# Kernel optimization log

Measured on AMD Instinct MI355X. Metric: run time of the kernel, lower is better.

The kernel has to match this reference:

```python
import jax, jax.numpy as jnp
import numpy as np

NUM_ROUTING = 3
EPS = 1e-7  # keras.backend.epsilon()


def squash(x, axis=-1):
    # squash(s) = (||s||^2 / (1 + ||s||^2)) * s / ||s||, stabilized
    n2 = jnp.sum(x * x, axis=axis, keepdims=True)
    return (n2 / (1.0 + n2)) * x / jnp.sqrt(n2 + EPS)


def setup_inputs() -> dict:
    key = jax.random.key(0)
    k1, k2 = jax.random.split(key)
    B, N_IN, N_OUT, D = 32, 2048, 64, 16
    inputs = jax.random.normal(k1, (B, N_IN, N_OUT, D), dtype=jnp.float32)
    bias = jax.random.normal(k2, (N_OUT, D), dtype=jnp.float32) * 0.01
    return {"inputs": inputs, "bias": bias}


def reference(inputs, bias):
    # inputs: [b, n_in, n_out, d_out]; bias: [n_out, d_out]
    priors = jnp.zeros_like(inputs)
    outputs = None
    for i in range(NUM_ROUTING):
        agreements = jax.nn.softmax(priors, axis=2)           # over n_out
        outputs = jnp.sum(inputs * agreements, axis=1, keepdims=True)  # [b,1,n_out,d]
        outputs = squash(outputs + bias)                       # activation='linear' -> plain squash
        if i < NUM_ROUTING - 1:
            # agreement update, broadcast over d_out
            priors = priors + jnp.sum(inputs * outputs, axis=-1, keepdims=True)
    # reduce '... n_in n_out d_out -> ... n_out d_out' (n_in axis has size 1 here)
    return jnp.sum(outputs, axis=1)
```

## Files before the change

### kernel.cpp

```cpp
#include <hip/hip_runtime.h>
#include <math.h>

#define BB 32
#define NIN 2048
#define NOUT 64
#define DD 16
#define CH 16
#define RPC 128
#define TPB 512

typedef float    f4 __attribute__((ext_vector_type(4)));
typedef float    f8 __attribute__((ext_vector_type(8)));
typedef _Float16 h4 __attribute__((ext_vector_type(4)));
typedef _Float16 h8 __attribute__((ext_vector_type(8)));

__device__ __forceinline__ float dot8(f8 a, f8 b) {
    float s01 = fmaf(a[1], b[1], a[0] * b[0]);
    float s23 = fmaf(a[3], b[3], a[2] * b[2]);
    float s45 = fmaf(a[5], b[5], a[4] * b[4]);
    float s67 = fmaf(a[7], b[7], a[6] * b[6]);
    return (s01 + s23) + (s45 + s67);
}

__global__ __launch_bounds__(TPB, 4) void pass0_kernel(
    const float* __restrict__ x, h4* __restrict__ xh, f4* __restrict__ pout)
{
    const int blk  = blockIdx.x;
    const int chunk = blk & (CH - 1);
    const int b    = blk >> 4;
    const int tid  = threadIdx.x;
    const int lane = tid & 63, wave = tid >> 6;

    f4 acc[4];
    #pragma unroll
    for (int j = 0; j < 4; ++j) acc[j] = f4{0.f, 0.f, 0.f, 0.f};

    const size_t row0 = (size_t)b * NIN + (size_t)chunk * RPC;

    #pragma unroll 2
    for (int r = wave; r < RPC; r += 8) {
        const f4* rp = (const f4*)x + (row0 + r) * 256;
        h4* hp = xh + (row0 + r) * 256;
        #pragma unroll
        for (int j = 0; j < 4; ++j) {
            f4 xv = __builtin_nontemporal_load(&rp[j * 64 + lane]);
            acc[j] += xv;
            hp[j * 64 + lane] = __builtin_convertvector(xv, h4);
        }
    }

    __shared__ f4 red[8][256];
    #pragma unroll
    for (int j = 0; j < 4; ++j) red[wave][j * 64 + lane] = acc[j];
    __syncthreads();
    if (tid < 256) {
        f4 s = red[0][tid];
        #pragma unroll
        for (int w = 1; w < 8; ++w) s += red[w][tid];
        pout[((size_t)(b * CH + chunk)) * 256 + tid] = s;
    }
}

__device__ __forceinline__ void compute_v(
    const f4* __restrict__ pin, const float* __restrict__ bias,
    int b, int tid, float scale, float* vsm, float* vout, int dowrite)
{
    if (tid < 256) {
        f4 s = pin[((size_t)b * CH) * 256 + tid];
        #pragma unroll
        for (int c = 1; c < CH; ++c) s += pin[((size_t)(b * CH + c)) * 256 + tid];
        const f4 bi = ((const f4*)bias)[tid];
        s = s * scale + bi;
        float n2 = s.x * s.x + s.y * s.y + s.z * s.z + s.w * s.w;
        n2 += __shfl_xor(n2, 1);
        n2 += __shfl_xor(n2, 2);
        const float k = n2 / ((1.0f + n2) * sqrtf(n2 + 1e-7f));
        const f4 v = s * k;
        *(f4*)(vsm + tid * 4) = v;
        if (dowrite) ((f4*)vout)[b * 256 + tid] = v;
    }
    __syncthreads();
}

template <int MODE>
__global__ __launch_bounds__(TPB, 4) void pass_kernel(
    const h8* __restrict__ xh,
    const f4* __restrict__ pin,
    const float* __restrict__ bias,
    const float* __restrict__ v0g,
    float* __restrict__ v0out,
    f4* __restrict__ pout)
{
    const int blk  = blockIdx.x;
    const int chunk = blk & (CH - 1);
    const int b    = blk >> 4;
    const int tid  = threadIdx.x;
    const int lane = tid & 63, wave = tid >> 6;

    __shared__ __align__(32) float vsm[1024];
    __shared__ __align__(32) float wsm[1024];
    __shared__ f4 red[8][256];

    const size_t row0 = (size_t)b * NIN + (size_t)chunk * RPC;

    const h8* hp0 = xh + (row0 + wave) * 128;
    h8 hx0 = hp0[lane];
    h8 hx1 = hp0[64 + lane];

    if (MODE == 1) {
        compute_v(pin, bias, b, tid, 1.0f / 64.0f, vsm, v0out, chunk == 0);
    } else {
        if (tid < 256) *(f4*)(vsm + tid * 4) = ((const f4*)v0g)[b * 256 + tid];
        compute_v(pin, bias, b, tid, 1.0f, wsm, nullptr, 0);
    }

    f8 vaf[2];
    #pragma unroll
    for (int j = 0; j < 2; ++j) {
        const int idx = j * 64 + lane;
        vaf[j] = *(const f8*)(vsm + idx * 8);
        if (MODE == 2) vaf[j] += *(const f8*)(wsm + idx * 8);
    }

    f8 acc0 = {0.f, 0.f, 0.f, 0.f, 0.f, 0.f, 0.f, 0.f};
    f8 acc1 = acc0;

    #pragma unroll 2
    for (int r = wave; r < RPC; r += 8) {
        const f8 x0 = __builtin_convertvector(hx0, f8);
        const f8 x1 = __builtin_convertvector(hx1, f8);
        if (r + 8 < RPC) {
            const h8* np = xh + (row0 + r + 8) * 128;
            hx0 = np[lane];
            hx1 = np[64 + lane];
        }

        float d0 = dot8(x0, vaf[0]);
        float d1 = dot8(x1, vaf[1]);
        d0 += __shfl_xor(d0, 1);
        d1 += __shfl_xor(d1, 1);

        const float e0 = __expf(d0), e1 = __expf(d1);
        float p = e0 + e1;
        #pragma unroll
        for (int o = 2; o <= 32; o <<= 1) p += __shfl_xor(p, o);
        const float inv = __builtin_amdgcn_rcpf(p);
        const float a0 = e0 * inv, a1 = e1 * inv;
        #pragma unroll
        for (int k = 0; k < 8; ++k) acc0[k] = fmaf(x0[k], a0, acc0[k]);
        #pragma unroll
        for (int k = 0; k < 8; ++k) acc1[k] = fmaf(x1[k], a1, acc1[k]);
    }

    *(f8*)(&red[wave][lane * 2])       = acc0;
    *(f8*)(&red[wave][128 + lane * 2]) = acc1;
    __syncthreads();
    if (tid < 256) {
        f4 s = red[0][tid];
        #pragma unroll
        for (int w = 1; w < 8; ++w) s += red[w][tid];
        pout[((size_t)(b * CH + chunk)) * 256 + tid] = s;
    }
}

__global__ __launch_bounds__(256) void finish_kernel(
    const f4* __restrict__ pin, const float* __restrict__ bias, f4* __restrict__ out)
{
    const int b = blockIdx.x;
    const int tid = threadIdx.x;
    f4 s = pin[((size_t)b * CH) * 256 + tid];
    #pragma unroll
    for (int c = 1; c < CH; ++c) s += pin[((size_t)(b * CH + c)) * 256 + tid];
    s = s + ((const f4*)bias)[tid];
    float n2 = s.x * s.x + s.y * s.y + s.z * s.z + s.w * s.w;
    n2 += __shfl_xor(n2, 1);
    n2 += __shfl_xor(n2, 2);
    const float k = n2 / ((1.0f + n2) * sqrtf(n2 + 1e-7f));
    out[b * 256 + tid] = s * k;
}

extern "C" void kernel_launch(void* const* d_in, const int* in_sizes, int n_in,
                              void* d_out, int out_size, void* d_ws, size_t ws_size,
                              hipStream_t stream) {
    const float* x    = (const float*)d_in[0];
    const float* bias = (const float*)d_in[1];
    float* out        = (float*)d_out;

    const size_t XH_BYTES = (size_t)BB * NIN * 1024 * 2;
    h4*    xh = (h4*)d_ws;
    float* pA = (float*)((char*)d_ws + XH_BYTES);
    float* pB = pA + (size_t)BB * CH * 1024;
    float* pC = pB + (size_t)BB * CH * 1024;
    float* v0buf = pC + (size_t)BB * CH * 1024;

    pass0_kernel<<<BB * CH, TPB, 0, stream>>>(x, xh, (f4*)pA);
    pass_kernel<1><<<BB * CH, TPB, 0, stream>>>((const h8*)xh, (const f4*)pA, bias,
                                                nullptr, v0buf, (f4*)pB);
    pass_kernel<2><<<BB * CH, TPB, 0, stream>>>((const h8*)xh, (const f4*)pB, bias,
                                                v0buf, nullptr, (f4*)pC);
    finish_kernel<<<BB, 256, 0, stream>>>((const f4*)pC, bias, (f4*)out);
}
```

Before: 116.4 us.

## Split routing passes into two batch halves with smaller blocks for cache residency

Runs the three routing passes separately for each half of the batch (16 samples at a time). The aim is to keep that half's fp16 copy of the inputs (about 64 MB) resident in the last-level cache between passes. Blocks shrink to 256 threads with 64 rows each, and chunks per sample double to 32, giving more blocks per launch. In exchange there are twice as many kernel launches, and compute_v now sums twice as many partial results.

Measured after the change: 135.7 us. 1.17x slower.

```diff
diff --git a/kernel.cpp b/kernel.cpp
--- a/kernel.cpp
+++ b/kernel.cpp
@@ -2,12 +2,13 @@
 #include <math.h>
 
 #define BB 32
+#define HB 16
 #define NIN 2048
 #define NOUT 64
 #define DD 16
-#define CH 16
-#define RPC 128
-#define TPB 512
+#define CH 32
+#define RPC 64
+#define TPB 256
 
 typedef float    f4 __attribute__((ext_vector_type(4)));
 typedef float    f8 __attribute__((ext_vector_type(8)));
@@ -23,13 +24,13 @@
 }
 
 __global__ __launch_bounds__(TPB, 4) void pass0_kernel(
-    const float* __restrict__ x, h4* __restrict__ xh, f4* __restrict__ pout)
+    const float* __restrict__ x, h4* __restrict__ xh, f4* __restrict__ pout, int b0)
 {
-    const int blk  = blockIdx.x;
+    const int blk   = blockIdx.x;
     const int chunk = blk & (CH - 1);
-    const int b    = blk >> 4;
-    const int tid  = threadIdx.x;
-    const int lane = tid & 63, wave = tid >> 6;
+    const int b     = b0 + (blk >> 5);
+    const int tid   = threadIdx.x;
+    const int lane  = tid & 63, wave = tid >> 6;
 
     f4 acc[4];
     #pragma unroll
@@ -38,7 +39,7 @@
     const size_t row0 = (size_t)b * NIN + (size_t)chunk * RPC;
 
     #pragma unroll 2
-    for (int r = wave; r < RPC; r += 8) {
+    for (int r = wave; r < RPC; r += 4) {
         const f4* rp = (const f4*)x + (row0 + r) * 256;
         h4* hp = xh + (row0 + r) * 256;
         #pragma unroll
@@ -49,36 +50,30 @@
         }
     }
 
-    __shared__ f4 red[8][256];
+    __shared__ f4 red[4][256];
     #pragma unroll
     for (int j = 0; j < 4; ++j) red[wave][j * 64 + lane] = acc[j];
     __syncthreads();
-    if (tid < 256) {
-        f4 s = red[0][tid];
-        #pragma unroll
-        for (int w = 1; w < 8; ++w) s += red[w][tid];
-        pout[((size_t)(b * CH + chunk)) * 256 + tid] = s;
-    }
+    f4 s = (red[0][tid] + red[1][tid]) + (red[2][tid] + red[3][tid]);
+    pout[((size_t)(b * CH + chunk)) * 256 + tid] = s;
 }
 
 __device__ __forceinline__ void compute_v(
     const f4* __restrict__ pin, const float* __restrict__ bias,
     int b, int tid, float scale, float* vsm, float* vout, int dowrite)
 {
-    if (tid < 256) {
-        f4 s = pin[((size_t)b * CH) * 256 + tid];
-        #pragma unroll
-        for (int c = 1; c < CH; ++c) s += pin[((size_t)(b * CH + c)) * 256 + tid];
-        const f4 bi = ((const f4*)bias)[tid];
-        s = s * scale + bi;
-        float n2 = s.x * s.x + s.y * s.y + s.z * s.z + s.w * s.w;
-        n2 += __shfl_xor(n2, 1);
-        n2 += __shfl_xor(n2, 2);
-        const float k = n2 / ((1.0f + n2) * sqrtf(n2 + 1e-7f));
-        const f4 v = s * k;
-        *(f4*)(vsm + tid * 4) = v;
-        if (dowrite) ((f4*)vout)[b * 256 + tid] = v;
-    }
+    f4 s = pin[((size_t)b * CH) * 256 + tid];
+    #pragma unroll
+    for (int c = 1; c < CH; ++c) s += pin[((size_t)(b * CH + c)) * 256 + tid];
+    const f4 bi = ((const f4*)bias)[tid];
+    s = s * scale + bi;
+    float n2 = s.x * s.x + s.y * s.y + s.z * s.z + s.w * s.w;
+    n2 += __shfl_xor(n2, 1);
+    n2 += __shfl_xor(n2, 2);
+    const float k = n2 / ((1.0f + n2) * sqrtf(n2 + 1e-7f));
+    const f4 v = s * k;
+    *(f4*)(vsm + tid * 4) = v;
+    if (dowrite) ((f4*)vout)[b * 256 + tid] = v;
     __syncthreads();
 }
 
@@ -89,17 +84,17 @@
     const float* __restrict__ bias,
     const float* __restrict__ v0g,
     float* __restrict__ v0out,
-    f4* __restrict__ pout)
+    f4* __restrict__ pout, int b0)
 {
-    const int blk  = blockIdx.x;
+    const int blk   = blockIdx.x;
     const int chunk = blk & (CH - 1);
-    const int b    = blk >> 4;
-    const int tid  = threadIdx.x;
-    const int lane = tid & 63, wave = tid >> 6;
+    const int b     = b0 + (blk >> 5);
+    const int tid   = threadIdx.x;
+    const int lane  = tid & 63, wave = tid >> 6;
 
     __shared__ __align__(32) float vsm[1024];
     __shared__ __align__(32) float wsm[1024];
-    __shared__ f4 red[8][256];
+    __shared__ f4 red[4][256];
 
     const size_t row0 = (size_t)b * NIN + (size_t)chunk * RPC;
 
@@ -110,7 +105,7 @@
     if (MODE == 1) {
         compute_v(pin, bias, b, tid, 1.0f / 64.0f, vsm, v0out, chunk == 0);
     } else {
-        if (tid < 256) *(f4*)(vsm + tid * 4) = ((const f4*)v0g)[b * 256 + tid];
+        *(f4*)(vsm + tid * 4) = ((const f4*)v0g)[b * 256 + tid];
         compute_v(pin, bias, b, tid, 1.0f, wsm, nullptr, 0);
     }
 
@@ -126,11 +121,11 @@
     f8 acc1 = acc0;
 
     #pragma unroll 2
-    for (int r = wave; r < RPC; r += 8) {
+    for (int r = wave; r < RPC; r += 4) {
         const f8 x0 = __builtin_convertvector(hx0, f8);
         const f8 x1 = __builtin_convertvector(hx1, f8);
-        if (r + 8 < RPC) {
-            const h8* np = xh + (row0 + r + 8) * 128;
+        if (r + 4 < RPC) {
+            const h8* np = xh + (row0 + r + 4) * 128;
             hx0 = np[lane];
             hx1 = np[64 + lane];
         }
@@ -155,12 +150,8 @@
     *(f8*)(&red[wave][lane * 2])       = acc0;
     *(f8*)(&red[wave][128 + lane * 2]) = acc1;
     __syncthreads();
-    if (tid < 256) {
-        f4 s = red[0][tid];
-        #pragma unroll
-        for (int w = 1; w < 8; ++w) s += red[w][tid];
-        pout[((size_t)(b * CH + chunk)) * 256 + tid] = s;
-    }
+    f4 s = (red[0][tid] + red[1][tid]) + (red[2][tid] + red[3][tid]);
+    pout[((size_t)(b * CH + chunk)) * 256 + tid] = s;
 }
 
 __global__ __launch_bounds__(256) void finish_kernel(
@@ -193,10 +184,15 @@
     float* pC = pB + (size_t)BB * CH * 1024;
     float* v0buf = pC + (size_t)BB * CH * 1024;
 
-    pass0_kernel<<<BB * CH, TPB, 0, stream>>>(x, xh, (f4*)pA);
-    pass_kernel<1><<<BB * CH, TPB, 0, stream>>>((const h8*)xh, (const f4*)pA, bias,
-                                                nullptr, v0buf, (f4*)pB);
-    pass_kernel<2><<<BB * CH, TPB, 0, stream>>>((const h8*)xh, (const f4*)pB, bias,
-                                                v0buf, nullptr, (f4*)pC);
+    const int HGRID = HB * CH;
+
+    for (int h = 0; h < 2; ++h) {
+        const int b0 = h * HB;
+        pass0_kernel<<<HGRID, TPB, 0, stream>>>(x, xh, (f4*)pA, b0);
+        pass_kernel<1><<<HGRID, TPB, 0, stream>>>((const h8*)xh, (const f4*)pA, bias,
+                                                  nullptr, v0buf, (f4*)pB, b0);
+        pass_kernel<2><<<HGRID, TPB, 0, stream>>>((const h8*)xh, (const f4*)pB, bias,
+                                                  v0buf, nullptr, (f4*)pC, b0);
+    }
     finish_kernel<<<BB, 256, 0, stream>>>((const f4*)pC, bias, (f4*)out);
 }
```

## Fuse per-batch squash into last-block tail via atomic counters, drop finish kernel

Applied to the files above, without the earlier changes.

Each pass kernel now writes its partial sums with atomic stores and increments a per-batch counter, and the last-arriving block for that batch reduces all chunks, applies bias and squash, and writes v. This replaces the old scheme in which every block of the next kernel re-reduced all 16 partials redundantly, and it removes the separate finish kernel launch. In exchange it adds a memset launch, atomic traffic and a serialized tail on one block per batch.

Result: slower. 179.8 us (+54.5%).

```diff
diff --git a/kernel.cpp b/kernel.cpp
--- a/kernel.cpp
+++ b/kernel.cpp
@@ -3,16 +3,24 @@
 
 #define BB 32
 #define NIN 2048
-#define NOUT 64
-#define DD 16
 #define CH 16
 #define RPC 128
 #define TPB 512
+#define NW 8
 
 typedef float    f4 __attribute__((ext_vector_type(4)));
 typedef float    f8 __attribute__((ext_vector_type(8)));
 typedef _Float16 h4 __attribute__((ext_vector_type(4)));
 typedef _Float16 h8 __attribute__((ext_vector_type(8)));
+
+#define AS __HIP_MEMORY_SCOPE_AGENT
+
+__device__ __forceinline__ void ast(float* p, float v) {
+    __hip_atomic_store(p, v, __ATOMIC_RELAXED, AS);
+}
+__device__ __forceinline__ float ald(const float* p) {
+    return __hip_atomic_load((float*)p, __ATOMIC_RELAXED, AS);
+}
 
 __device__ __forceinline__ float dot8(f8 a, f8 b) {
     float s01 = fmaf(a[1], b[1], a[0] * b[0]);
@@ -22,13 +30,52 @@
     return (s01 + s23) + (s45 + s67);
 }
 
+__device__ __forceinline__ void tail_reduce(
+    f4* red, float* pX, int* cnt, const float* bias,
+    float* vdst, float scale, bool plainOut, int b, int blk, int tid)
+{
+    __syncthreads();
+    if (tid < 256) {
+        f4 s = (red[tid] + red[256 + tid]) + (red[512 + tid] + red[768 + tid]);
+        s += (red[1024 + tid] + red[1280 + tid]) + (red[1536 + tid] + red[1792 + tid]);
+        float* dst = pX + (size_t)blk * 1024 + tid * 4;
+        ast(dst, s.x); ast(dst + 1, s.y); ast(dst + 2, s.z); ast(dst + 3, s.w);
+    }
+    __syncthreads();
+    __shared__ int sLast;
+    if (tid == 0)
+        sLast = (__hip_atomic_fetch_add(&cnt[b], 1, __ATOMIC_ACQ_REL, AS) == CH - 1);
+    __syncthreads();
+    if (!sLast) return;
+
+    if (tid < 256) {
+        f4 t = f4{0.f, 0.f, 0.f, 0.f};
+        #pragma unroll 4
+        for (int c = 0; c < CH; ++c) {
+            const float* src = pX + (size_t)(b * CH + c) * 1024 + tid * 4;
+            t += f4{ald(src), ald(src + 1), ald(src + 2), ald(src + 3)};
+        }
+        t = t * scale + ((const f4*)bias)[tid];
+        float n2 = t.x * t.x + t.y * t.y + t.z * t.z + t.w * t.w;
+        n2 += __shfl_xor(n2, 1);
+        n2 += __shfl_xor(n2, 2);
+        const float kf = n2 / ((1.f + n2) * sqrtf(n2 + 1e-7f));
+        t *= kf;
+        float* d = vdst + (size_t)b * 1024 + tid * 4;
+        if (plainOut) *(f4*)d = t;
+        else { ast(d, t.x); ast(d + 1, t.y); ast(d + 2, t.z); ast(d + 3, t.w); }
+    }
+}
+
 __global__ __launch_bounds__(TPB, 4) void pass0_kernel(
-    const float* __restrict__ x, h4* __restrict__ xh, f4* __restrict__ pout)
+    const float* __restrict__ x, h4* __restrict__ xh,
+    float* __restrict__ pA, int* __restrict__ cnt0,
+    const float* __restrict__ bias, float* __restrict__ v0)
 {
-    const int blk  = blockIdx.x;
+    const int blk = blockIdx.x;
     const int chunk = blk & (CH - 1);
-    const int b    = blk >> 4;
-    const int tid  = threadIdx.x;
+    const int b = blk >> 4;
+    const int tid = threadIdx.x;
     const int lane = tid & 63, wave = tid >> 6;
 
     f4 acc[4];
@@ -38,7 +85,7 @@
     const size_t row0 = (size_t)b * NIN + (size_t)chunk * RPC;
 
     #pragma unroll 2
-    for (int r = wave; r < RPC; r += 8) {
+    for (int r = wave; r < RPC; r += NW) {
         const f4* rp = (const f4*)x + (row0 + r) * 256;
         h4* hp = xh + (row0 + r) * 256;
         #pragma unroll
@@ -49,57 +96,25 @@
         }
     }
 
-    __shared__ f4 red[8][256];
+    __shared__ f4 red[NW * 256];
     #pragma unroll
-    for (int j = 0; j < 4; ++j) red[wave][j * 64 + lane] = acc[j];
-    __syncthreads();
-    if (tid < 256) {
-        f4 s = red[0][tid];
-        #pragma unroll
-        for (int w = 1; w < 8; ++w) s += red[w][tid];
-        pout[((size_t)(b * CH + chunk)) * 256 + tid] = s;
-    }
-}
-
-__device__ __forceinline__ void compute_v(
-    const f4* __restrict__ pin, const float* __restrict__ bias,
-    int b, int tid, float scale, float* vsm, float* vout, int dowrite)
-{
-    if (tid < 256) {
-        f4 s = pin[((size_t)b * CH) * 256 + tid];
-        #pragma unroll
-        for (int c = 1; c < CH; ++c) s += pin[((size_t)(b * CH + c)) * 256 + tid];
-        const f4 bi = ((const f4*)bias)[tid];
-        s = s * scale + bi;
-        float n2 = s.x * s.x + s.y * s.y + s.z * s.z + s.w * s.w;
-        n2 += __shfl_xor(n2, 1);
-        n2 += __shfl_xor(n2, 2);
-        const float k = n2 / ((1.0f + n2) * sqrtf(n2 + 1e-7f));
-        const f4 v = s * k;
-        *(f4*)(vsm + tid * 4) = v;
-        if (dowrite) ((f4*)vout)[b * 256 + tid] = v;
-    }
-    __syncthreads();
+    for (int j = 0; j < 4; ++j) red[wave * 256 + j * 64 + lane] = acc[j];
+    tail_reduce(red, pA, cnt0, bias, v0, 1.0f / 64.0f, false, b, blk, tid);
 }
 
 template <int MODE>
 __global__ __launch_bounds__(TPB, 4) void pass_kernel(
     const h8* __restrict__ xh,
-    const f4* __restrict__ pin,
+    const float* __restrict__ v0g, const float* __restrict__ v1g,
     const float* __restrict__ bias,
-    const float* __restrict__ v0g,
-    float* __restrict__ v0out,
-    f4* __restrict__ pout)
+    float* __restrict__ pX, int* __restrict__ cnt,
+    float* __restrict__ vdst)
 {
-    const int blk  = blockIdx.x;
+    const int blk = blockIdx.x;
     const int chunk = blk & (CH - 1);
-    const int b    = blk >> 4;
-    const int tid  = threadIdx.x;
+    const int b = blk >> 4;
+    const int tid = threadIdx.x;
     const int lane = tid & 63, wave = tid >> 6;
-
-    __shared__ __align__(32) float vsm[1024];
-    __shared__ __align__(32) float wsm[1024];
-    __shared__ f4 red[8][256];
 
     const size_t row0 = (size_t)b * NIN + (size_t)chunk * RPC;
 
@@ -107,30 +122,23 @@
     h8 hx0 = hp0[lane];
     h8 hx1 = hp0[64 + lane];
 
-    if (MODE == 1) {
-        compute_v(pin, bias, b, tid, 1.0f / 64.0f, vsm, v0out, chunk == 0);
-    } else {
-        if (tid < 256) *(f4*)(vsm + tid * 4) = ((const f4*)v0g)[b * 256 + tid];
-        compute_v(pin, bias, b, tid, 1.0f, wsm, nullptr, 0);
-    }
-
     f8 vaf[2];
     #pragma unroll
     for (int j = 0; j < 2; ++j) {
         const int idx = j * 64 + lane;
-        vaf[j] = *(const f8*)(vsm + idx * 8);
-        if (MODE == 2) vaf[j] += *(const f8*)(wsm + idx * 8);
+        vaf[j] = *(const f8*)(v0g + (size_t)b * 1024 + idx * 8);
+        if (MODE == 2) vaf[j] += *(const f8*)(v1g + (size_t)b * 1024 + idx * 8);
     }
 
     f8 acc0 = {0.f, 0.f, 0.f, 0.f, 0.f, 0.f, 0.f, 0.f};
     f8 acc1 = acc0;
 
     #pragma unroll 2
-    for (int r = wave; r < RPC; r += 8) {
+    for (int r = wave; r < RPC; r += NW) {
         const f8 x0 = __builtin_convertvector(hx0, f8);
         const f8 x1 = __builtin_convertvector(hx1, f8);
-        if (r + 8 < RPC) {
-            const h8* np = xh + (row0 + r + 8) * 128;
+        if (r + NW < RPC) {
+            const h8* np = xh + (row0 + r + NW) * 128;
             hx0 = np[lane];
             hx1 = np[64 + lane];
         }
@@ -152,31 +160,10 @@
         for (int k = 0; k < 8; ++k) acc1[k] = fmaf(x1[k], a1, acc1[k]);
     }
 
-    *(f8*)(&red[wave][lane * 2])       = acc0;
-    *(f8*)(&red[wave][128 + lane * 2]) = acc1;
-    __syncthreads();
-    if (tid < 256) {
-        f4 s = red[0][tid];
-        #pragma unroll
-        for (int w = 1; w < 8; ++w) s += red[w][tid];
-        pout[((size_t)(b * CH + chunk)) * 256 + tid] = s;
-    }
-}
-
-__global__ __launch_bounds__(256) void finish_kernel(
-    const f4* __restrict__ pin, const float* __restrict__ bias, f4* __restrict__ out)
-{
-    const int b = blockIdx.x;
-    const int tid = threadIdx.x;
-    f4 s = pin[((size_t)b * CH) * 256 + tid];
-    #pragma unroll
-    for (int c = 1; c < CH; ++c) s += pin[((size_t)(b * CH + c)) * 256 + tid];
-    s = s + ((const f4*)bias)[tid];
-    float n2 = s.x * s.x + s.y * s.y + s.z * s.z + s.w * s.w;
-    n2 += __shfl_xor(n2, 1);
-    n2 += __shfl_xor(n2, 2);
-    const float k = n2 / ((1.0f + n2) * sqrtf(n2 + 1e-7f));
-    out[b * 256 + tid] = s * k;
+    __shared__ f4 red[NW * 256];
+    *(f8*)(&red[wave * 256 + lane * 2])       = acc0;
+    *(f8*)(&red[wave * 256 + 128 + lane * 2]) = acc1;
+    tail_reduce(red, pX, cnt, bias, vdst, 1.0f, MODE == 2, b, blk, tid);
 }
 
 extern "C" void kernel_launch(void* const* d_in, const int* in_sizes, int n_in,
@@ -185,18 +172,24 @@
     const float* x    = (const float*)d_in[0];
     const float* bias = (const float*)d_in[1];
     float* out        = (float*)d_out;
+    char* wsb         = (char*)d_ws;
 
-    const size_t XH_BYTES = (size_t)BB * NIN * 1024 * 2;
-    h4*    xh = (h4*)d_ws;
-    float* pA = (float*)((char*)d_ws + XH_BYTES);
-    float* pB = pA + (size_t)BB * CH * 1024;
-    float* pC = pB + (size_t)BB * CH * 1024;
-    float* v0buf = pC + (size_t)BB * CH * 1024;
+    int*   cnt0 = (int*)(wsb + 0);
+    int*   cnt1 = (int*)(wsb + 128);
+    int*   cnt2 = (int*)(wsb + 256);
+    float* v0   = (float*)(wsb + 1024);
+    float* v1   = v0 + BB * 1024;
+    float* pA   = v1 + BB * 1024;
+    float* pB   = pA + (size_t)BB * CH * 1024;
+    float* pC   = pB + (size_t)BB * CH * 1024;
+    h4*    xh   = (h4*)(pC + (size_t)BB * CH * 1024);
 
-    pass0_kernel<<<BB * CH, TPB, 0, stream>>>(x, xh, (f4*)pA);
-    pass_kernel<1><<<BB * CH, TPB, 0, stream>>>((const h8*)xh, (const f4*)pA, bias,
-                                                nullptr, v0buf, (f4*)pB);
-    pass_kernel<2><<<BB * CH, TPB, 0, stream>>>((const h8*)xh, (const f4*)pB, bias,
-                                                v0buf, nullptr, (f4*)pC);
-    finish_kernel<<<BB, 256, 0, stream>>>((const f4*)pC, bias, (f4*)out);
+    hipMemsetAsync(wsb, 0, 1024, stream);
+
+    const int GRID = BB * CH;
+    pass0_kernel<<<GRID, TPB, 0, stream>>>(x, xh, pA, cnt0, bias, v0);
+    pass_kernel<1><<<GRID, TPB, 0, stream>>>((const h8*)xh, v0, nullptr, bias,
+                                             pB, cnt1, v1);
+    pass_kernel<2><<<GRID, TPB, 0, stream>>>((const h8*)xh, v0, v1, bias,
+                                             pC, cnt2, out);
 }
```
